# Kernel tuning notes

Measured on AMD Instinct MI355X. Metric: run time of the kernel, lower is better.

Reference implementation:

```python
import jax, jax.numpy as jnp
import numpy as np

L, D_IN, D, H, FF, C = 6, 64, 512, 8, 2048, 5
HD = D // H
LN_EPS = 1e-5


def _ln(x, g, b):
    mu = jnp.mean(x, axis=-1, keepdims=True)
    var = jnp.mean((x - mu) ** 2, axis=-1, keepdims=True)
    return (x - mu) * jax.lax.rsqrt(var + LN_EPS) * g + b


def setup_inputs() -> dict:
    key = jax.random.key(0)
    ks = iter(jax.random.split(key, 64))
    s = 0.02

    def w(shape):
        return (jax.random.normal(next(ks), shape, dtype=jnp.float32) * s)

    inp = {
        "src": jax.random.normal(next(ks), (8, 1024, D_IN), dtype=jnp.float32),
        "key_padding_mask": jnp.zeros((8, 1024), dtype=bool),
        "embed_W": w((D, D_IN)), "embed_b": jnp.zeros((D,), jnp.float32),
        # stacked per-layer params (torch Linear convention: W is [out, in])
        "Wq": w((L, D, D)), "bq": jnp.zeros((L, D), jnp.float32),
        "Wk": w((L, D, D)), "bk": jnp.zeros((L, D), jnp.float32),
        "Wv": w((L, D, D)), "bv": jnp.zeros((L, D), jnp.float32),
        "Wo": w((L, D, D)), "bo": jnp.zeros((L, D), jnp.float32),
        "W1": w((L, FF, D)), "b1": jnp.zeros((L, FF), jnp.float32),
        "W2": w((L, D, FF)), "b2": jnp.zeros((L, D), jnp.float32),
        "ln1_g": jnp.ones((L, D), jnp.float32), "ln1_b": jnp.zeros((L, D), jnp.float32),
        "ln2_g": jnp.ones((L, D), jnp.float32), "ln2_b": jnp.zeros((L, D), jnp.float32),
        "fin_g": jnp.ones((D,), jnp.float32), "fin_b": jnp.zeros((D,), jnp.float32),
        "head_W": w((C, D)), "head_b": jnp.zeros((C,), jnp.float32),
    }
    return inp


def reference(src, key_padding_mask, embed_W, embed_b, Wq, bq, Wk, bk, Wv, bv,
              Wo, bo, W1, b1, W2, b2, ln1_g, ln1_b, ln2_g, ln2_b,
              fin_g, fin_b, head_W, head_b):
    B, N, _ = src.shape
    x = src @ embed_W.T + embed_b  # [B, N, D]
    neg_inf = jnp.float32(-jnp.inf)
    kpm = key_padding_mask[:, None, None, :]  # [B,1,1,N]

    def layer(x, p):
        (wq, bq_, wk, bk_, wv, bv_, wo, bo_,
         w1, b1_, w2, b2_, g1, be1, g2, be2) = p
        q = (x @ wq.T + bq_).reshape(B, N, H, HD).transpose(0, 2, 1, 3)
        k = (x @ wk.T + bk_).reshape(B, N, H, HD).transpose(0, 2, 1, 3)
        v = (x @ wv.T + bv_).reshape(B, N, H, HD).transpose(0, 2, 1, 3)
        scores = jnp.einsum('bhqd,bhkd->bhqk', q, k) / jnp.sqrt(jnp.float32(HD))
        scores = jnp.where(kpm, neg_inf, scores)
        probs = jax.nn.softmax(scores + 1e-9, axis=-1)
        attn = jnp.einsum('bhqk,bhkd->bhqd', probs, v)
        attn = attn.transpose(0, 2, 1, 3).reshape(B, N, D) @ wo.T + bo_
        x = _ln(x + attn, g1, be1)  # post-norm (norm_first=False)
        ff = jax.nn.relu(x @ w1.T + b1_) @ w2.T + b2_
        x = _ln(x + ff, g2, be2)
        return x, None

    params = (Wq, bq, Wk, bk, Wv, bv, Wo, bo, W1, b1, W2, b2,
              ln1_g, ln1_b, ln2_g, ln2_b)
    x, _ = jax.lax.scan(layer, x, params)
    x = _ln(x, fin_g, fin_b)  # encoder_norm (norm_first=False branch)
    logits = x @ head_W.T + head_b  # [B, N, C]
    return logits
```

## Files before the change

### kernel.cpp

```cpp
#include <hip/hip_runtime.h>
#include <hip/hip_bf16.h>
#include <math.h>

#define B_   8
#define NSEQ 1024
#define T_   (B_*NSEQ)
#define DIN  64
#define D_   512
#define H_   8
#define HD_  64
#define FF_  2048
#define L_   6
#define C_   5

typedef __attribute__((ext_vector_type(8))) short bf16x8;
typedef __attribute__((ext_vector_type(4))) float f32x4;

__device__ __forceinline__ unsigned short f2bf(float f) {
    __hip_bfloat16 h = __float2bfloat16(f);
    return *reinterpret_cast<unsigned short*>(&h);
}
__device__ __forceinline__ float bf2f(unsigned short u) {
    __hip_bfloat16 h = *reinterpret_cast<__hip_bfloat16*>(&u);
    return __bfloat162float(h);
}

__device__ __forceinline__ void gload_lds16(const void* g, void* l) {
    __builtin_amdgcn_global_load_lds(
        (const __attribute__((address_space(1))) unsigned int*)g,
        (__attribute__((address_space(3))) unsigned int*)l, 16, 0, 0);
}

template<bool RELU, int BN>
__global__ __launch_bounds__(256, BN==64 ? 3 : 2)
void gemm_mfma_kernel(const unsigned short* __restrict__ A,
                      const unsigned short* __restrict__ W,
                      const float* __restrict__ bias,
                      unsigned short* __restrict__ Cout,
                      int M, int N, int K)
{
    constexpr int BM = 128, BK = 64;
    constexpr int NFN = BN/32;
    __shared__ short As[2][BM*BK];
    __shared__ short Bs[2][BN*BK];
    const int tid = threadIdx.x;
    const int l   = tid & 63;
    const int wid = tid >> 6;
    const int wm  = wid >> 1, wn = wid & 1;

    const int gx  = gridDim.x;
    const int nwg = gx * gridDim.y;
    int bid = blockIdx.y * gx + blockIdx.x;
    bid = (bid & 7) * (nwg >> 3) + (bid >> 3);
    const int bm = (bid / gx) * BM;
    const int bn = (bid % gx) * BN;

    const int srow = l >> 3;
    const int scol = ((l & 7) ^ srow) * 8;

    f32x4 acc[4][NFN];
    const f32x4 z = {0.f, 0.f, 0.f, 0.f};
    #pragma unroll
    for (int m = 0; m < 4; m++)
        #pragma unroll
        for (int n = 0; n < NFN; n++) acc[m][n] = z;

    const int nk = K / BK;

    auto stage = [&](int kt, int sb) {
        const int k0 = kt * BK;
        #pragma unroll
        for (int c = 0; c < 4; c++) {
            const int r = wid*32 + c*8 + srow;
            gload_lds16(A + (size_t)(bm + r)*K + k0 + scol, &As[sb][(wid*32 + c*8)*64]);
        }
        #pragma unroll
        for (int c = 0; c < BN/32; c++) {
            const int r = wid*(BN/4) + c*8 + srow;
            gload_lds16(W + (size_t)(bn + r)*K + k0 + scol, &Bs[sb][(wid*(BN/4) + c*8)*64]);
        }
    };

    stage(0, 0);
    int buf = 0;
    for (int kt = 0; kt < nk; kt++) {
        __syncthreads();
        if (kt + 1 < nk) stage(kt + 1, buf ^ 1);

        #pragma unroll
        for (int h = 0; h < 2; h++) {
            bf16x8 af[4], bfr[NFN];
            #pragma unroll
            for (int m = 0; m < 4; m++) {
                const int R  = wm*64 + m*16 + (l & 15);
                const int cb = (h*64 + (l >> 4)*16) ^ ((R & 7) << 4);
                af[m] = *(const bf16x8*)((const char*)&As[buf][0] + R*128 + cb);
            }
            #pragma unroll
            for (int n = 0; n < NFN; n++) {
                const int Rc = wn*(BN/2) + n*16 + (l & 15);
                const int cb = (h*64 + (l >> 4)*16) ^ ((Rc & 7) << 4);
                bfr[n] = *(const bf16x8*)((const char*)&Bs[buf][0] + Rc*128 + cb);
            }
            #pragma unroll
            for (int m = 0; m < 4; m++)
                #pragma unroll
                for (int n = 0; n < NFN; n++)
                    acc[m][n] = __builtin_amdgcn_mfma_f32_16x16x32_bf16(af[m], bfr[n], acc[m][n], 0, 0, 0);
        }
        buf ^= 1;
    }

    #pragma unroll
    for (int n = 0; n < NFN; n++) {
        const int col = bn + wn*(BN/2) + n*16 + (l & 15);
        const float bv = bias[col];
        #pragma unroll
        for (int m = 0; m < 4; m++) {
            const int row0 = bm + wm*64 + m*16 + ((l >> 4) << 2);
            #pragma unroll
            for (int j = 0; j < 4; j++) {
                float t = acc[m][n][j] + bv;
                if (RELU) t = fmaxf(t, 0.f);
                Cout[(size_t)(row0 + j)*N + col] = f2bf(t);
            }
        }
    }
}

__global__ __launch_bounds__(256, 2)
void attn_mfma_kernel(const unsigned short* __restrict__ QKV,
                      const unsigned char* __restrict__ mask,
                      unsigned short* __restrict__ O)
{
    constexpr int QS = 1536;
    constexpr float CEXP = 0.18033688f;
    __shared__ short Ks[2][64*64];
    __shared__ short Vt[2][64*72];
    __shared__ short Ps[4][32*72];
    const int tid = threadIdx.x;
    const int l   = tid & 63;
    const int w   = tid >> 6;
    const int g   = l >> 4;
    const int q16 = l & 15;
    const int b   = blockIdx.y >> 3;
    const int h   = blockIdx.y & 7;
    const int q0  = blockIdx.x * 128;
    const int qb  = q0 + w*32;
    const size_t tokbase = (size_t)b * NSEQ;

    bf16x8 bq[2][2];
    #pragma unroll
    for (int qf = 0; qf < 2; qf++) {
        const unsigned short* qp = QKV + (tokbase + qb + qf*16 + q16)*QS + h*HD_ + g*8;
        bq[qf][0] = *(const bf16x8*)qp;
        bq[qf][1] = *(const bf16x8*)(qp + 32);
    }

    f32x4 accO[2][4];
    const f32x4 z = {0.f,0.f,0.f,0.f};
    #pragma unroll
    for (int qf = 0; qf < 2; qf++)
        #pragma unroll
        for (int n = 0; n < 4; n++) accO[qf][n] = z;
    float mrow[2] = {-INFINITY, -INFINITY};
    float lrow[2] = {0.f, 0.f};

    const int srow = l >> 3;
    const int scol = ((l & 7) ^ srow) * 8;
    const unsigned char* mp = mask + (size_t)b*NSEQ;

    #pragma unroll
    for (int c = 0; c < 2; c++) {
        const int rb = (w*2 + c)*8;
        gload_lds16(QKV + (tokbase + rb + srow)*QS + D_ + h*HD_ + scol, &Ks[0][rb*64]);
    }
    {
        const unsigned short* vp = QKV + (tokbase + l)*QS + 2*D_ + h*HD_ + w*16;
        const bf16x8 v8a = *(const bf16x8*)vp;
        const bf16x8 v8b = *(const bf16x8*)(vp + 8);
        #pragma unroll
        for (int j = 0; j < 8; j++) {
            Vt[0][(w*16 + j)*72 + l]     = v8a[j];
            Vt[0][(w*16 + 8 + j)*72 + l] = v8b[j];
        }
    }

    for (int t = 0; t < NSEQ/64; t++) {
        const int buf = t & 1;
        const int kv0 = t*64;
        __syncthreads();

        bf16x8 nva, nvb;
        const bool more = (t + 1 < NSEQ/64);
        if (more) {
            const int kvn = kv0 + 64;
            #pragma unroll
            for (int c = 0; c < 2; c++) {
                const int rb = (w*2 + c)*8;
                gload_lds16(QKV + (tokbase + kvn + rb + srow)*QS + D_ + h*HD_ + scol,
                            &Ks[buf^1][rb*64]);
            }
            const unsigned short* vp = QKV + (tokbase + kvn + l)*QS + 2*D_ + h*HD_ + w*16;
            nva = *(const bf16x8*)vp;
            nvb = *(const bf16x8*)(vp + 8);
        }

        f32x4 s4[2][4];
        #pragma unroll
        for (int qf = 0; qf < 2; qf++)
            #pragma unroll
            for (int n = 0; n < 4; n++) s4[qf][n] = z;
        __builtin_amdgcn_s_setprio(1);
        #pragma unroll
        for (int ks = 0; ks < 2; ks++) {
            const int cb = (ks*64 + g*16) ^ ((q16 & 7) << 4);
            bf16x8 ak[4];
            #pragma unroll
            for (int n = 0; n < 4; n++)
                ak[n] = *(const bf16x8*)((const char*)&Ks[buf][0] + (n*16 + q16)*128 + cb);
            #pragma unroll
            for (int qf = 0; qf < 2; qf++)
                #pragma unroll
                for (int n = 0; n < 4; n++)
                    s4[qf][n] = __builtin_amdgcn_mfma_f32_16x16x32_bf16(ak[n], bq[qf][ks], s4[qf][n], 0, 0, 0);
        }
        __builtin_amdgcn_s_setprio(0);

        const unsigned long long mbits = __ballot(mp[kv0 + l] != 0);

        #pragma unroll
        for (int qf = 0; qf < 2; qf++) {
            float sv[4][4];
            #pragma unroll
            for (int n = 0; n < 4; n++)
                #pragma unroll
                for (int r = 0; r < 4; r++) sv[n][r] = s4[qf][n][r];
            if (mbits) {
                #pragma unroll
                for (int n = 0; n < 4; n++)
                    #pragma unroll
                    for (int r = 0; r < 4; r++)
                        if ((mbits >> (unsigned)(16*n + 4*g + r)) & 1ULL) sv[n][r] = -INFINITY;
            }
            float tmax = sv[0][0];
            #pragma unroll
            for (int n = 0; n < 4; n++)
                #pragma unroll
                for (int r = 0; r < 4; r++) tmax = fmaxf(tmax, sv[n][r]);
            tmax = fmaxf(tmax, __shfl_xor(tmax, 16));
            tmax = fmaxf(tmax, __shfl_xor(tmax, 32));

            unsigned int pw[4][2];
            float rs = 0.f;
            if (__all(tmax <= mrow[qf] + 64.f)) {
                const float mc = mrow[qf]*CEXP;
                #pragma unroll
                for (int n = 0; n < 4; n++) {
                    const float p0 = exp2f(fmaf(sv[n][0], CEXP, -mc));
                    const float p1 = exp2f(fmaf(sv[n][1], CEXP, -mc));
                    const float p2 = exp2f(fmaf(sv[n][2], CEXP, -mc));
                    const float p3 = exp2f(fmaf(sv[n][3], CEXP, -mc));
                    pw[n][0] = (unsigned)f2bf(p0) | ((unsigned)f2bf(p1) << 16);
                    pw[n][1] = (unsigned)f2bf(p2) | ((unsigned)f2bf(p3) << 16);
                    rs += (p0 + p1) + (p2 + p3);
                }
                rs += __shfl_xor(rs, 16);
                rs += __shfl_xor(rs, 32);
                lrow[qf] += rs;
            } else {
                const float mnew = fmaxf(mrow[qf], tmax);
                const float mc   = mnew*CEXP;
                #pragma unroll
                for (int n = 0; n < 4; n++) {
                    const float p0 = exp2f(fmaf(sv[n][0], CEXP, -mc));
                    const float p1 = exp2f(fmaf(sv[n][1], CEXP, -mc));
                    const float p2 = exp2f(fmaf(sv[n][2], CEXP, -mc));
                    const float p3 = exp2f(fmaf(sv[n][3], CEXP, -mc));
                    pw[n][0] = (unsigned)f2bf(p0) | ((unsigned)f2bf(p1) << 16);
                    pw[n][1] = (unsigned)f2bf(p2) | ((unsigned)f2bf(p3) << 16);
                    rs += (p0 + p1) + (p2 + p3);
                }
                rs += __shfl_xor(rs, 16);
                rs += __shfl_xor(rs, 32);
                const float alpha = exp2f((mrow[qf] - mnew)*CEXP);
                lrow[qf] = lrow[qf]*alpha + rs;
                mrow[qf] = mnew;
                float alr[4];
                #pragma unroll
                for (int r = 0; r < 4; r++) alr[r] = __shfl(alpha, g*4 + r, 16);
                #pragma unroll
                for (int n = 0; n < 4; n++)
                    #pragma unroll
                    for (int r = 0; r < 4; r++) accO[qf][n][r] *= alr[r];
            }

            #pragma unroll
            for (int n = 0; n < 4; n++) {
                uint2 u; u.x = pw[n][0]; u.y = pw[n][1];
                *(uint2*)&Ps[w][(qf*16 + q16)*72 + 16*n + 4*g] = u;
            }
        }

        __builtin_amdgcn_s_setprio(1);
        #pragma unroll
        for (int ks = 0; ks < 2; ks++) {
            const bf16x8 ap0 = *(const bf16x8*)&Ps[w][(q16)*72      + ks*32 + g*8];
            const bf16x8 ap1 = *(const bf16x8*)&Ps[w][(16 + q16)*72 + ks*32 + g*8];
            #pragma unroll
            for (int n = 0; n < 4; n++) {
                const bf16x8 bv = *(const bf16x8*)&Vt[buf][(n*16 + q16)*72 + ks*32 + g*8];
                accO[0][n] = __builtin_amdgcn_mfma_f32_16x16x32_bf16(ap0, bv, accO[0][n], 0, 0, 0);
                accO[1][n] = __builtin_amdgcn_mfma_f32_16x16x32_bf16(ap1, bv, accO[1][n], 0, 0, 0);
            }
        }
        __builtin_amdgcn_s_setprio(0);

        if (more) {
            #pragma unroll
            for (int j = 0; j < 8; j++) {
                Vt[buf^1][(w*16 + j)*72 + l]     = nva[j];
                Vt[buf^1][(w*16 + 8 + j)*72 + l] = nvb[j];
            }
        }
    }

    #pragma unroll
    for (int qf = 0; qf < 2; qf++) {
        float linv[4];
        #pragma unroll
        for (int r = 0; r < 4; r++) linv[r] = 1.0f / __shfl(lrow[qf], g*4 + r, 16);
        #pragma unroll
        for (int r = 0; r < 4; r++) {
            unsigned short* op = O + (tokbase + qb + qf*16 + 4*g + r)*D_ + h*HD_;
            #pragma unroll
            for (int n = 0; n < 4; n++)
                op[16*n + q16] = f2bf(accO[qf][n][r] * linv[r]);
        }
    }
}

__global__ __launch_bounds__(256)
void add_ln_kernel(unsigned short* __restrict__ x,
                   const unsigned short* __restrict__ delta,
                   const float* __restrict__ g, const float* __restrict__ bta)
{
    const int lane = threadIdx.x & 63;
    const int row  = blockIdx.x*4 + (threadIdx.x >> 6);
    unsigned short* xr = x + (size_t)row*D_ + lane*8;
    const bf16x8 xv8 = *(const bf16x8*)xr;
    const bf16x8 dv8 = *(const bf16x8*)(delta + (size_t)row*D_ + lane*8);
    float v[8], sum = 0.f, sq = 0.f;
    #pragma unroll
    for (int j = 0; j < 8; j++) {
        v[j] = bf2f((unsigned short)xv8[j]) + bf2f((unsigned short)dv8[j]);
        sum += v[j];
        sq  = fmaf(v[j], v[j], sq);
    }
    #pragma unroll
    for (int off = 1; off < 64; off <<= 1) {
        sum += __shfl_xor(sum, off, 64);
        sq  += __shfl_xor(sq,  off, 64);
    }
    const float mu  = sum * (1.f/D_);
    const float var = sq * (1.f/D_) - mu*mu;
    const float rs  = rsqrtf(var + 1e-5f);
    const float4 g0 = *(const float4*)(g + lane*8);
    const float4 g1 = *(const float4*)(g + lane*8 + 4);
    const float4 b0 = *(const float4*)(bta + lane*8);
    const float4 b1 = *(const float4*)(bta + lane*8 + 4);
    const float gf[8] = {g0.x,g0.y,g0.z,g0.w,g1.x,g1.y,g1.z,g1.w};
    const float bf_[8] = {b0.x,b0.y,b0.z,b0.w,b1.x,b1.y,b1.z,b1.w};
    bf16x8 o;
    #pragma unroll
    for (int j = 0; j < 8; j++)
        o[j] = (short)f2bf(fmaf((v[j] - mu)*rs, gf[j], bf_[j]));
    *(bf16x8*)xr = o;
}

__global__ __launch_bounds__(256)
void ln_head_kernel(const unsigned short* __restrict__ x,
                    const float* __restrict__ g, const float* __restrict__ bta,
                    const float* __restrict__ hw, const float* __restrict__ hb,
                    float* __restrict__ out)
{
    const int lane = threadIdx.x & 63;
    const int row  = blockIdx.x*4 + (threadIdx.x >> 6);
    const bf16x8 xv8 = *(const bf16x8*)(x + (size_t)row*D_ + lane*8);
    float v[8], sum = 0.f, sq = 0.f;
    #pragma unroll
    for (int j = 0; j < 8; j++) {
        v[j] = bf2f((unsigned short)xv8[j]);
        sum += v[j];
        sq  = fmaf(v[j], v[j], sq);
    }
    #pragma unroll
    for (int off = 1; off < 64; off <<= 1) {
        sum += __shfl_xor(sum, off, 64);
        sq  += __shfl_xor(sq,  off, 64);
    }
    const float mu  = sum * (1.f/D_);
    const float var = sq * (1.f/D_) - mu*mu;
    const float rs  = rsqrtf(var + 1e-5f);
    const float4 g0 = *(const float4*)(g + lane*8);
    const float4 g1 = *(const float4*)(g + lane*8 + 4);
    const float4 b0 = *(const float4*)(bta + lane*8);
    const float4 b1 = *(const float4*)(bta + lane*8 + 4);
    const float gf[8] = {g0.x,g0.y,g0.z,g0.w,g1.x,g1.y,g1.z,g1.w};
    const float bf_[8] = {b0.x,b0.y,b0.z,b0.w,b1.x,b1.y,b1.z,b1.w};
    float o[8];
    #pragma unroll
    for (int j = 0; j < 8; j++)
        o[j] = fmaf((v[j] - mu)*rs, gf[j], bf_[j]);

    float part[C_];
    #pragma unroll
    for (int c = 0; c < C_; c++) {
        const float4 w0 = *(const float4*)(hw + c*D_ + lane*8);
        const float4 w1 = *(const float4*)(hw + c*D_ + lane*8 + 4);
        part[c] = o[0]*w0.x + o[1]*w0.y + o[2]*w0.z + o[3]*w0.w
                + o[4]*w1.x + o[5]*w1.y + o[6]*w1.z + o[7]*w1.w;
    }
    #pragma unroll
    for (int c = 0; c < C_; c++)
        #pragma unroll
        for (int off = 1; off < 64; off <<= 1)
            part[c] += __shfl_xor(part[c], off, 64);
    if (lane == 0) {
        #pragma unroll
        for (int c = 0; c < C_; c++)
            out[(size_t)row*C_ + c] = part[c] + hb[c];
    }
}

__global__ __launch_bounds__(256)
void cast_bf16_kernel(const float* __restrict__ in, unsigned short* __restrict__ out, int n)
{
    const int i = (blockIdx.x*256 + threadIdx.x)*4;
    if (i < n) {
        const float4 v = *(const float4*)(in + i);
        ushort4 o;
        o.x = f2bf(v.x); o.y = f2bf(v.y); o.z = f2bf(v.z); o.w = f2bf(v.w);
        *(ushort4*)(out + i) = o;
    }
}

__global__ __launch_bounds__(256)
void cast_qkv_kernel(const float* __restrict__ Wq, const float* __restrict__ Wk,
                     const float* __restrict__ Wv, unsigned short* __restrict__ dst)
{
    const int t  = blockIdx.y;
    const int ll = t / 3, wh = t % 3;
    const int DD = D_*D_;
    const float* srcs[3] = {Wq, Wk, Wv};
    const float* src = srcs[wh] + (size_t)ll*DD;
    unsigned short* d = dst + (size_t)ll*3*DD + (size_t)wh*DD;
    const int i = (blockIdx.x*256 + threadIdx.x)*4;
    if (i < DD) {
        const float4 v = *(const float4*)(src + i);
        ushort4 o;
        o.x = f2bf(v.x); o.y = f2bf(v.y); o.z = f2bf(v.z); o.w = f2bf(v.w);
        *(ushort4*)(d + i) = o;
    }
}

__global__ __launch_bounds__(256)
void qkv_bias_kernel(const float* __restrict__ bq, const float* __restrict__ bk,
                     const float* __restrict__ bv, float* __restrict__ dst)
{
    const int idx = blockIdx.x*256 + threadIdx.x;
    const int ll = idx / 1536, c = idx % 1536;
    float v;
    if (c < 512)       v = bq[ll*512 + c];
    else if (c < 1024) v = bk[ll*512 + c - 512];
    else               v = bv[ll*512 + c - 1024];
    dst[idx] = v;
}

extern "C" void kernel_launch(void* const* d_in, const int* in_sizes, int n_in,
                              void* d_out, int out_size, void* d_ws, size_t ws_size,
                              hipStream_t stream)
{
    const float* src     = (const float*)d_in[0];
    const unsigned char* kpm = (const unsigned char*)d_in[1];
    const float* embed_W = (const float*)d_in[2];
    const float* embed_b = (const float*)d_in[3];
    const float* Wq = (const float*)d_in[4];
    const float* bq = (const float*)d_in[5];
    const float* Wk = (const float*)d_in[6];
    const float* bk = (const float*)d_in[7];
    const float* Wv = (const float*)d_in[8];
    const float* bv = (const float*)d_in[9];
    const float* Wo = (const float*)d_in[10];
    const float* bo = (const float*)d_in[11];
    const float* W1 = (const float*)d_in[12];
    const float* b1 = (const float*)d_in[13];
    const float* W2 = (const float*)d_in[14];
    const float* b2 = (const float*)d_in[15];
    const float* ln1_g = (const float*)d_in[16];
    const float* ln1_b = (const float*)d_in[17];
    const float* ln2_g = (const float*)d_in[18];
    const float* ln2_b = (const float*)d_in[19];
    const float* fin_g = (const float*)d_in[20];
    const float* fin_b = (const float*)d_in[21];
    const float* head_W = (const float*)d_in[22];
    const float* head_b = (const float*)d_in[23];
    float* out = (float*)d_out;

    const size_t S = (size_t)T_ * D_;
    unsigned short* u16  = (unsigned short*)d_ws;
    unsigned short* xb   = u16;
    unsigned short* qkvb = u16 + 1*S;
    unsigned short* attb = u16 + 4*S;
    unsigned short* tmpb = u16 + 5*S;
    unsigned short* h1b  = u16 + 1*S;
    unsigned short* wb   = u16 + 6*S;
    const int DD = D_*D_;
    const int DF = D_*FF_;
    unsigned short* wqkvb = wb;
    unsigned short* wob   = wb + 18*(size_t)DD;
    unsigned short* w1b   = wb + 24*(size_t)DD;
    unsigned short* w2b   = wb + 48*(size_t)DD;
    float* qkvbias        = (float*)(wb + 72*(size_t)DD);
    unsigned short* srcb  = (unsigned short*)(qkvbias + 6*1536);
    unsigned short* embWb = srcb + (size_t)T_*DIN;

    const dim3 blk(256);
    const dim3 gQKV(1536/128, T_/128);
    const dim3 gN512(D_/64,   T_/128);
    const dim3 gMF (FF_/128,  T_/128);

    cast_qkv_kernel<<<dim3(DD/1024, 18), blk, 0, stream>>>(Wq, Wk, Wv, wqkvb);
    cast_bf16_kernel<<<6*DD/1024, blk, 0, stream>>>(Wo, wob, 6*DD);
    cast_bf16_kernel<<<6*DF/1024, blk, 0, stream>>>(W1, w1b, 6*DF);
    cast_bf16_kernel<<<6*DF/1024, blk, 0, stream>>>(W2, w2b, 6*DF);
    qkv_bias_kernel<<<(6*1536)/256, blk, 0, stream>>>(bq, bk, bv, qkvbias);
    cast_bf16_kernel<<<T_*DIN/1024, blk, 0, stream>>>(src, srcb, T_*DIN);
    cast_bf16_kernel<<<D_*DIN/1024, blk, 0, stream>>>(embed_W, embWb, D_*DIN);

    gemm_mfma_kernel<false,64><<<gN512, blk, 0, stream>>>(srcb, embWb, embed_b, xb, T_, D_, DIN);

    for (int l = 0; l < L_; l++) {
        const float* bol = bo + (size_t)l*D_;
        const float* b1l = b1 + (size_t)l*FF_;
        const float* b2l = b2 + (size_t)l*D_;

        gemm_mfma_kernel<false,128><<<gQKV, blk, 0, stream>>>(xb, wqkvb + (size_t)l*3*DD,
                                                              qkvbias + (size_t)l*1536, qkvb, T_, 1536, D_);

        attn_mfma_kernel<<<dim3(NSEQ/128, B_*H_), blk, 0, stream>>>(qkvb, kpm, attb);

        gemm_mfma_kernel<false,64><<<gN512, blk, 0, stream>>>(attb, wob + (size_t)l*DD, bol, tmpb, T_, D_, D_);
        add_ln_kernel<<<T_/4, blk, 0, stream>>>(xb, tmpb, ln1_g + (size_t)l*D_, ln1_b + (size_t)l*D_);

        gemm_mfma_kernel<true ,128><<<gMF, blk, 0, stream>>>(xb, w1b + (size_t)l*DF, b1l, h1b, T_, FF_, D_);
        gemm_mfma_kernel<false,64><<<gN512, blk, 0, stream>>>(h1b, w2b + (size_t)l*DF, b2l, tmpb, T_, D_, FF_);
        add_ln_kernel<<<T_/4, blk, 0, stream>>>(xb, tmpb, ln2_g + (size_t)l*D_, ln2_b + (size_t)l*D_);
    }

    ln_head_kernel<<<T_/4, blk, 0, stream>>>(xb, fin_g, fin_b, head_W, head_b, out);
}
```

Measured before the change: 1.051 ms.

## Single-buffer GEMM LDS for higher occupancy and remap attention block order

```diff
diff --git a/kernel.cpp b/kernel.cpp
--- a/kernel.cpp
+++ b/kernel.cpp
@@ -32,7 +32,7 @@
 }
 
 template<bool RELU, int BN>
-__global__ __launch_bounds__(256, BN==64 ? 3 : 2)
+__global__ __launch_bounds__(256, 3)
 void gemm_mfma_kernel(const unsigned short* __restrict__ A,
                       const unsigned short* __restrict__ W,
                       const float* __restrict__ bias,
@@ -41,8 +41,8 @@
 {
     constexpr int BM = 128, BK = 64;
     constexpr int NFN = BN/32;
-    __shared__ short As[2][BM*BK];
-    __shared__ short Bs[2][BN*BK];
+    __shared__ short As[BM*BK];
+    __shared__ short Bs[BN*BK];
     const int tid = threadIdx.x;
     const int l   = tid & 63;
     const int wid = tid >> 6;
@@ -66,26 +66,20 @@
         for (int n = 0; n < NFN; n++) acc[m][n] = z;
 
     const int nk = K / BK;
-
-    auto stage = [&](int kt, int sb) {
+    for (int kt = 0; kt < nk; kt++) {
         const int k0 = kt * BK;
+        __syncthreads();
         #pragma unroll
         for (int c = 0; c < 4; c++) {
             const int r = wid*32 + c*8 + srow;
-            gload_lds16(A + (size_t)(bm + r)*K + k0 + scol, &As[sb][(wid*32 + c*8)*64]);
+            gload_lds16(A + (size_t)(bm + r)*K + k0 + scol, &As[(wid*32 + c*8)*64]);
         }
         #pragma unroll
         for (int c = 0; c < BN/32; c++) {
             const int r = wid*(BN/4) + c*8 + srow;
-            gload_lds16(W + (size_t)(bn + r)*K + k0 + scol, &Bs[sb][(wid*(BN/4) + c*8)*64]);
-        }
-    };
-
-    stage(0, 0);
-    int buf = 0;
-    for (int kt = 0; kt < nk; kt++) {
+            gload_lds16(W + (size_t)(bn + r)*K + k0 + scol, &Bs[(wid*(BN/4) + c*8)*64]);
+        }
         __syncthreads();
-        if (kt + 1 < nk) stage(kt + 1, buf ^ 1);
 
         #pragma unroll
         for (int h = 0; h < 2; h++) {
@@ -94,13 +88,13 @@
             for (int m = 0; m < 4; m++) {
                 const int R  = wm*64 + m*16 + (l & 15);
                 const int cb = (h*64 + (l >> 4)*16) ^ ((R & 7) << 4);
-                af[m] = *(const bf16x8*)((const char*)&As[buf][0] + R*128 + cb);
+                af[m] = *(const bf16x8*)((const char*)As + R*128 + cb);
             }
             #pragma unroll
             for (int n = 0; n < NFN; n++) {
                 const int Rc = wn*(BN/2) + n*16 + (l & 15);
                 const int cb = (h*64 + (l >> 4)*16) ^ ((Rc & 7) << 4);
-                bfr[n] = *(const bf16x8*)((const char*)&Bs[buf][0] + Rc*128 + cb);
+                bfr[n] = *(const bf16x8*)((const char*)Bs + Rc*128 + cb);
             }
             #pragma unroll
             for (int m = 0; m < 4; m++)
@@ -108,7 +102,6 @@
                 for (int n = 0; n < NFN; n++)
                     acc[m][n] = __builtin_amdgcn_mfma_f32_16x16x32_bf16(af[m], bfr[n], acc[m][n], 0, 0, 0);
         }
-        buf ^= 1;
     }
 
     #pragma unroll
@@ -143,9 +136,13 @@
     const int w   = tid >> 6;
     const int g   = l >> 4;
     const int q16 = l & 15;
-    const int b   = blockIdx.y >> 3;
-    const int h   = blockIdx.y & 7;
-    const int q0  = blockIdx.x * 128;
+
+    const int j   = blockIdx.y * gridDim.x + blockIdx.x;
+    const int qi  = (j >> 3) & 7;
+    const int bh  = ((j >> 6) << 3) | (j & 7);
+    const int b   = bh >> 3;
+    const int h   = bh & 7;
+    const int q0  = qi * 128;
     const int qb  = q0 + w*32;
     const size_t tokbase = (size_t)b * NSEQ;
 
@@ -180,9 +177,9 @@
         const bf16x8 v8a = *(const bf16x8*)vp;
         const bf16x8 v8b = *(const bf16x8*)(vp + 8);
         #pragma unroll
-        for (int j = 0; j < 8; j++) {
-            Vt[0][(w*16 + j)*72 + l]     = v8a[j];
-            Vt[0][(w*16 + 8 + j)*72 + l] = v8b[j];
+        for (int jj = 0; jj < 8; jj++) {
+            Vt[0][(w*16 + jj)*72 + l]     = v8a[jj];
+            Vt[0][(w*16 + 8 + jj)*72 + l] = v8b[jj];
         }
     }
 
@@ -318,9 +315,9 @@
 
         if (more) {
             #pragma unroll
-            for (int j = 0; j < 8; j++) {
-                Vt[buf^1][(w*16 + j)*72 + l]     = nva[j];
-                Vt[buf^1][(w*16 + 8 + j)*72 + l] = nvb[j];
+            for (int jj = 0; jj < 8; jj++) {
+                Vt[buf^1][(w*16 + jj)*72 + l]     = nva[jj];
+                Vt[buf^1][(w*16 + 8 + jj)*72 + l] = nvb[jj];
             }
         }
     }
```

New measurement: 988.4 us. 5.9% less time.
